# Kernel optimization log

Measured on AMD Instinct MI355X. Metric: run time of the kernel, lower is better.

Reference implementation:

```python
import jax, jax.numpy as jnp
import numpy as np

N_NODES = 40000
N_EDGES = 640000
D_FEAT = 128


def setup_inputs() -> dict:
    key = jax.random.key(0)
    k1, k2, k3, k4 = jax.random.split(key, 4)
    rows = jax.random.randint(k1, (N_EDGES,), 0, N_NODES, dtype=jnp.int32)
    cols = jax.random.randint(k2, (N_EDGES,), 0, N_NODES, dtype=jnp.int32)
    vals = jax.random.uniform(k3, (N_EDGES,), dtype=jnp.float32)
    annotations = jax.random.normal(k4, (N_NODES, D_FEAT), dtype=jnp.float32)
    return {"rows": rows, "cols": cols, "vals": vals, "annotations": annotations}


def reference(rows, cols, vals, annotations):
    # out = adjacent @ annotations, with adjacent given in COO form:
    # adjacent[rows[e], cols[e]] = vals[e].
    # SpMM as gather -> scale -> segment_sum over destination rows.
    gathered = annotations[cols] * vals[:, None]          # [E, d]
    out = jax.ops.segment_sum(gathered, rows, num_segments=N_NODES)  # [N, d]
    return out
```

## Files before the change

kernel.cpp:

```cpp
#include <hip/hip_runtime.h>


constexpr int N_NODES = 40000;
constexpr int N_EDGES = 640000;
constexpr int D_FEAT  = 128;
constexpr int CAP     = 32;
constexpr int OVF_CAP = 16384;

constexpr size_t WS_CURSOR = 0;
constexpr size_t WS_OVFCNT = 160000;
constexpr size_t WS_OVF    = 160256;
constexpr size_t WS_ANNB   = 422400;
constexpr size_t WS_PAIRS  = 10662400;
constexpr size_t WS_NEEDED = 20902400;

__device__ __forceinline__ unsigned f2b_rne(float f) {
    unsigned b = __float_as_uint(f);
    return (b + 0x7fffu + ((b >> 16) & 1u)) >> 16;
}

__global__ __launch_bounds__(256) void convert_kernel(
    const float* __restrict__ ann, uint2* __restrict__ annb)
{
    int t = blockIdx.x * blockDim.x + threadIdx.x;
    if (t < N_NODES * D_FEAT / 4) {
        float4 f = reinterpret_cast<const float4*>(ann)[t];
        uint2 o;
        o.x = f2b_rne(f.x) | (f2b_rne(f.y) << 16);
        o.y = f2b_rne(f.z) | (f2b_rne(f.w) << 16);
        annb[t] = o;
    }
}

__device__ __forceinline__ void scatter_one(
    int r, int c, float v, int* cursor, int2* pairs,
    int* ovfcnt, int4* ovf)
{
    int slot = atomicAdd(&cursor[r], 1);
    if (slot < CAP) {
        pairs[r * CAP + slot] = make_int2(c, __float_as_int(v));
    } else {
        int o = atomicAdd(ovfcnt, 1);
        if (o < OVF_CAP) ovf[o] = make_int4(r, c, __float_as_int(v), 0);
    }
}

__global__ __launch_bounds__(256) void scatter_kernel(
    const int*   __restrict__ rows,
    const int*   __restrict__ cols,
    const float* __restrict__ vals,
    int* __restrict__ cursor, int2* __restrict__ pairs,
    int* __restrict__ ovfcnt, int4* __restrict__ ovf)
{
    int t = blockIdx.x * blockDim.x + threadIdx.x;
    if (t < N_EDGES / 4) {
        int4   r4 = reinterpret_cast<const int4*>(rows)[t];
        int4   c4 = reinterpret_cast<const int4*>(cols)[t];
        float4 v4 = reinterpret_cast<const float4*>(vals)[t];
        scatter_one(r4.x, c4.x, v4.x, cursor, pairs, ovfcnt, ovf);
        scatter_one(r4.y, c4.y, v4.y, cursor, pairs, ovfcnt, ovf);
        scatter_one(r4.z, c4.z, v4.z, cursor, pairs, ovfcnt, ovf);
        scatter_one(r4.w, c4.w, v4.w, cursor, pairs, ovfcnt, ovf);
    }
}

__global__ __launch_bounds__(256) void pull_kernel(
    const unsigned* __restrict__ annb,
    const int*      __restrict__ cursor,
    const int2*     __restrict__ pairs,
    float*          __restrict__ out)
{
    int r    = (blockIdx.x * blockDim.x + threadIdx.x) >> 6;
    int lane = threadIdx.x & 63;
    if (r >= N_NODES) return;

    int cnt = cursor[r];
    cnt = cnt > CAP ? CAP : cnt;

    int2 pr = make_int2(0, 0);
    if (lane < cnt) pr = pairs[r * CAP + lane];

    float2 acc = make_float2(0.f, 0.f);
    int nb = (cnt + 7) & ~7;
    for (int j = 0; j < nb; j += 8) {
        #pragma unroll
        for (int k = 0; k < 8; k++) {
            int      c = __shfl(pr.x, j + k, 64);
            float    v = __int_as_float(__shfl(pr.y, j + k, 64));
            unsigned p = annb[c * (D_FEAT / 2) + lane];
            float a0 = __uint_as_float(p << 16);
            float a1 = __uint_as_float(p & 0xffff0000u);
            acc.x += v * a0;
            acc.y += v * a1;
        }
    }
    ((float2*)out)[(size_t)r * (D_FEAT / 2) + lane] = acc;
}

__global__ __launch_bounds__(256) void post_kernel(
    const float* __restrict__ ann,
    const int*   __restrict__ ovfcnt,
    const int4*  __restrict__ ovf,
    float*       __restrict__ out)
{
    int gid  = blockIdx.x * blockDim.x + threadIdx.x;
    int h    = gid >> 5;
    int lane = gid & 31;
    int n = *ovfcnt;
    n = n > OVF_CAP ? OVF_CAP : n;
    const int n_halves = (gridDim.x * blockDim.x) >> 5;
    for (int i = h; i < n; i += n_halves) {
        int4  e = ovf[i];
        float v = __int_as_float(e.z);
        float4 a = reinterpret_cast<const float4*>(ann)[(size_t)e.y * (D_FEAT / 4) + lane];
        float* o = out + (size_t)e.x * D_FEAT + lane * 4;
        unsafeAtomicAdd(o + 0, v * a.x);
        unsafeAtomicAdd(o + 1, v * a.y);
        unsafeAtomicAdd(o + 2, v * a.z);
        unsafeAtomicAdd(o + 3, v * a.w);
    }
}

__global__ __launch_bounds__(256) void spmm_scatter_kernel(
    const int*   __restrict__ rows,
    const int*   __restrict__ cols,
    const float* __restrict__ vals,
    const float* __restrict__ ann,
    float*       __restrict__ out)
{
    int t = blockIdx.x * blockDim.x + threadIdx.x;
    int e = t >> 5;
    if (e >= N_EDGES) return;
    int lane = t & 31;
    int   r = rows[e];
    int   c = cols[e];
    float v = vals[e];
    float4 a = reinterpret_cast<const float4*>(ann)[(size_t)c * (D_FEAT / 4) + lane];
    float* o = out + (size_t)r * D_FEAT + lane * 4;
    unsafeAtomicAdd(o + 0, v * a.x);
    unsafeAtomicAdd(o + 1, v * a.y);
    unsafeAtomicAdd(o + 2, v * a.z);
    unsafeAtomicAdd(o + 3, v * a.w);
}

extern "C" void kernel_launch(void* const* d_in, const int* in_sizes, int n_in,
                              void* d_out, int out_size, void* d_ws, size_t ws_size,
                              hipStream_t stream) {
    const int*   rows = (const int*)  d_in[0];
    const int*   cols = (const int*)  d_in[1];
    const float* vals = (const float*)d_in[2];
    const float* ann  = (const float*)d_in[3];
    float*       out  = (float*)      d_out;

    if (ws_size < WS_NEEDED) {
        hipMemsetAsync(out, 0, (size_t)out_size * sizeof(float), stream);
        const long long total_threads = (long long)N_EDGES * 32;
        spmm_scatter_kernel<<<dim3((unsigned)((total_threads + 255) / 256)),
                              dim3(256), 0, stream>>>(rows, cols, vals, ann, out);
        return;
    }

    char*     ws     = (char*)d_ws;
    int*      cursor = (int*)     (ws + WS_CURSOR);
    int*      ovfcnt = (int*)     (ws + WS_OVFCNT);
    int4*     ovf    = (int4*)    (ws + WS_OVF);
    unsigned* annb   = (unsigned*)(ws + WS_ANNB);
    int2*     pairs  = (int2*)    (ws + WS_PAIRS);

    hipMemsetAsync(cursor, 0, WS_OVF, stream);

    convert_kernel<<<dim3((N_NODES * D_FEAT / 4 + 255) / 256), dim3(256), 0, stream>>>(
        ann, (uint2*)annb);
    scatter_kernel<<<dim3((N_EDGES / 4 + 255) / 256), dim3(256), 0, stream>>>(
        rows, cols, vals, cursor, pairs, ovfcnt, ovf);

    const long long pull_threads = (long long)N_NODES * 64;
    pull_kernel<<<dim3((unsigned)((pull_threads + 255) / 256)), dim3(256), 0, stream>>>(
        annb, cursor, pairs, out);

    post_kernel<<<dim3(32), dim3(256), 0, stream>>>(ann, ovfcnt, ovf, out);
}
```

Baseline: 140.5 us.

## Fold cursor reset into convert and overflow pass into pull kernel

Drops the workspace memset by zeroing the cursor and overflow counter inside the convert kernel. Removes the separate post kernel by having pull wavefronts whose row overflowed scan the overflow list and add matching entries themselves. It also switches the streaming loads and stores to nontemporal builtins. The goal is fewer launches and less cache pollution. The cost is a linear scan of the overflow list for each overflowing row, which could be expensive if many rows overflow.

```diff
diff --git a/kernel.cpp b/kernel.cpp
--- a/kernel.cpp
+++ b/kernel.cpp
@@ -14,17 +14,25 @@
 constexpr size_t WS_PAIRS  = 10662400;
 constexpr size_t WS_NEEDED = 20902400;
 
+typedef int   v2i __attribute__((ext_vector_type(2)));
+typedef float v2f __attribute__((ext_vector_type(2)));
+typedef int   v4i __attribute__((ext_vector_type(4)));
+typedef float v4f __attribute__((ext_vector_type(4)));
+
 __device__ __forceinline__ unsigned f2b_rne(float f) {
     unsigned b = __float_as_uint(f);
     return (b + 0x7fffu + ((b >> 16) & 1u)) >> 16;
 }
 
 __global__ __launch_bounds__(256) void convert_kernel(
-    const float* __restrict__ ann, uint2* __restrict__ annb)
+    const float* __restrict__ ann, uint2* __restrict__ annb,
+    int* __restrict__ cursor, int* __restrict__ ovfcnt)
 {
     int t = blockIdx.x * blockDim.x + threadIdx.x;
+    if (t < N_NODES) cursor[t] = 0;
+    if (t == 0) *ovfcnt = 0;
     if (t < N_NODES * D_FEAT / 4) {
-        float4 f = reinterpret_cast<const float4*>(ann)[t];
+        v4f f = __builtin_nontemporal_load(reinterpret_cast<const v4f*>(ann) + t);
         uint2 o;
         o.x = f2b_rne(f.x) | (f2b_rne(f.y) << 16);
         o.y = f2b_rne(f.z) | (f2b_rne(f.w) << 16);
@@ -33,12 +41,15 @@
 }
 
 __device__ __forceinline__ void scatter_one(
-    int r, int c, float v, int* cursor, int2* pairs,
+    int r, int c, float v, int* cursor, v2i* pairs,
     int* ovfcnt, int4* ovf)
 {
     int slot = atomicAdd(&cursor[r], 1);
     if (slot < CAP) {
-        pairs[r * CAP + slot] = make_int2(c, __float_as_int(v));
+        v2i p;
+        p.x = c;
+        p.y = __float_as_int(v);
+        __builtin_nontemporal_store(p, pairs + (r * CAP + slot));
     } else {
         int o = atomicAdd(ovfcnt, 1);
         if (o < OVF_CAP) ovf[o] = make_int4(r, c, __float_as_int(v), 0);
@@ -49,14 +60,14 @@
     const int*   __restrict__ rows,
     const int*   __restrict__ cols,
     const float* __restrict__ vals,
-    int* __restrict__ cursor, int2* __restrict__ pairs,
+    int* __restrict__ cursor, v2i* __restrict__ pairs,
     int* __restrict__ ovfcnt, int4* __restrict__ ovf)
 {
     int t = blockIdx.x * blockDim.x + threadIdx.x;
     if (t < N_EDGES / 4) {
-        int4   r4 = reinterpret_cast<const int4*>(rows)[t];
-        int4   c4 = reinterpret_cast<const int4*>(cols)[t];
-        float4 v4 = reinterpret_cast<const float4*>(vals)[t];
+        v4i r4 = __builtin_nontemporal_load(reinterpret_cast<const v4i*>(rows) + t);
+        v4i c4 = __builtin_nontemporal_load(reinterpret_cast<const v4i*>(cols) + t);
+        v4f v4 = __builtin_nontemporal_load(reinterpret_cast<const v4f*>(vals) + t);
         scatter_one(r4.x, c4.x, v4.x, cursor, pairs, ovfcnt, ovf);
         scatter_one(r4.y, c4.y, v4.y, cursor, pairs, ovfcnt, ovf);
         scatter_one(r4.z, c4.z, v4.z, cursor, pairs, ovfcnt, ovf);
@@ -67,18 +78,24 @@
 __global__ __launch_bounds__(256) void pull_kernel(
     const unsigned* __restrict__ annb,
     const int*      __restrict__ cursor,
-    const int2*     __restrict__ pairs,
+    const v2i*      __restrict__ pairs,
+    const int*      __restrict__ ovfcnt,
+    const int4*     __restrict__ ovf,
     float*          __restrict__ out)
 {
     int r    = (blockIdx.x * blockDim.x + threadIdx.x) >> 6;
     int lane = threadIdx.x & 63;
     if (r >= N_NODES) return;
 
-    int cnt = cursor[r];
-    cnt = cnt > CAP ? CAP : cnt;
+    int cntr = cursor[r];
+    int cnt  = cntr > CAP ? CAP : cntr;
 
     int2 pr = make_int2(0, 0);
-    if (lane < cnt) pr = pairs[r * CAP + lane];
+    if (lane < cnt) {
+        v2i p = __builtin_nontemporal_load(pairs + (r * CAP + lane));
+        pr.x = p.x;
+        pr.y = p.y;
+    }
 
     float2 acc = make_float2(0.f, 0.f);
     int nb = (cnt + 7) & ~7;
@@ -94,31 +111,26 @@
             acc.y += v * a1;
         }
     }
-    ((float2*)out)[(size_t)r * (D_FEAT / 2) + lane] = acc;
-}
 
-__global__ __launch_bounds__(256) void post_kernel(
-    const float* __restrict__ ann,
-    const int*   __restrict__ ovfcnt,
-    const int4*  __restrict__ ovf,
-    float*       __restrict__ out)
-{
-    int gid  = blockIdx.x * blockDim.x + threadIdx.x;
-    int h    = gid >> 5;
-    int lane = gid & 31;
-    int n = *ovfcnt;
-    n = n > OVF_CAP ? OVF_CAP : n;
-    const int n_halves = (gridDim.x * blockDim.x) >> 5;
-    for (int i = h; i < n; i += n_halves) {
-        int4  e = ovf[i];
-        float v = __int_as_float(e.z);
-        float4 a = reinterpret_cast<const float4*>(ann)[(size_t)e.y * (D_FEAT / 4) + lane];
-        float* o = out + (size_t)e.x * D_FEAT + lane * 4;
-        unsafeAtomicAdd(o + 0, v * a.x);
-        unsafeAtomicAdd(o + 1, v * a.y);
-        unsafeAtomicAdd(o + 2, v * a.z);
-        unsafeAtomicAdd(o + 3, v * a.w);
+    if (cntr > CAP) {
+        int n = *ovfcnt;
+        n = n > OVF_CAP ? OVF_CAP : n;
+        for (int i = 0; i < n; i++) {
+            int4 e = ovf[i];
+            if (e.x == r) {
+                unsigned p = annb[e.y * (D_FEAT / 2) + lane];
+                float    v = __int_as_float(e.z);
+                acc.x += v * __uint_as_float(p << 16);
+                acc.y += v * __uint_as_float(p & 0xffff0000u);
+            }
+        }
     }
+
+    v2f o;
+    o.x = acc.x;
+    o.y = acc.y;
+    __builtin_nontemporal_store(
+        o, reinterpret_cast<v2f*>(out) + ((size_t)r * (D_FEAT / 2) + lane));
 }
 
 __global__ __launch_bounds__(256) void spmm_scatter_kernel(
@@ -165,18 +177,15 @@
     int*      ovfcnt = (int*)     (ws + WS_OVFCNT);
     int4*     ovf    = (int4*)    (ws + WS_OVF);
     unsigned* annb   = (unsigned*)(ws + WS_ANNB);
-    int2*     pairs  = (int2*)    (ws + WS_PAIRS);
-
-    hipMemsetAsync(cursor, 0, WS_OVF, stream);
+    v2i*      pairs  = (v2i*)     (ws + WS_PAIRS);
 
     convert_kernel<<<dim3((N_NODES * D_FEAT / 4 + 255) / 256), dim3(256), 0, stream>>>(
-        ann, (uint2*)annb);
+        ann, (uint2*)annb, cursor, ovfcnt);
+
     scatter_kernel<<<dim3((N_EDGES / 4 + 255) / 256), dim3(256), 0, stream>>>(
         rows, cols, vals, cursor, pairs, ovfcnt, ovf);
 
     const long long pull_threads = (long long)N_NODES * 64;
     pull_kernel<<<dim3((unsigned)((pull_threads + 255) / 256)), dim3(256), 0, stream>>>(
-        annb, cursor, pairs, out);
-
-    post_kernel<<<dim3(32), dim3(256), 0, stream>>>(ann, ovfcnt, ovf, out);
+        annb, cursor, pairs, ovfcnt, ovf, out);
 }
```

Measured after the change: 149.1 us. +6.1%, slower.
